# Kernel tuning notes

Measured on AMD Instinct MI355X. Metric: run time of the kernel, lower is better.

Reference implementation:

```python
import jax, jax.numpy as jnp
import numpy as np


def _coord1d(n):
    # make_coord: grid-center coordinates in (-1, 1)
    return -1.0 + 1.0 / n + (2.0 / n) * jnp.arange(n, dtype=jnp.float32)


def _conv1x1(x, w, b):
    # 1x1 conv == channel matmul. x: [B,C,H,W], w: [O,C], b: [O]
    return jnp.einsum('bchw,oc->bohw', x, w) + b[None, :, None, None]


def setup_inputs() -> dict:
    key = jax.random.key(0)
    ks = jax.random.split(key, 8)
    B, C, h, w = 2, 64, 96, 96
    d = 256
    Cin = (C + 2) * 4 + 2  # 266
    s = lambda k, shp, fan: (jax.random.normal(k, shp, jnp.float32) / np.sqrt(fan)).astype(jnp.float32)
    return {
        'feat': jax.random.normal(ks[0], (B, C, h, w), jnp.float32),
        'w00': s(ks[1], (d, Cin), Cin), 'b00': jnp.zeros((d,), jnp.float32),
        'w1': s(ks[2], (d, d), d), 'b1': jnp.zeros((d,), jnp.float32),
        'w2': s(ks[3], (3, d), d), 'b2': jnp.zeros((3,), jnp.float32),
        'ws1': s(ks[4], (C, C), C), 'bs1': jnp.zeros((C,), jnp.float32),
        'ws2': s(ks[5], (3, C), C), 'bs2': jnp.zeros((3,), jnp.float32),
        'target_h': 384, 'target_w': 384,
    }


def reference(feat, w00, b00, w1, b1, w2, b2, ws1, bs1, ws2, bs2, target_h, target_w):
    B, C, h, w = feat.shape
    H, W = int(target_h), int(target_w)
    # HR query coordinates, shared across batch. cy along height (dim0), cx along width (dim1)
    cy = jnp.broadcast_to(_coord1d(H)[:, None], (H, W))
    cx = jnp.broadcast_to(_coord1d(W)[None, :], (H, W))
    rx = 1.0 / h  # = 2/h/2, half-pixel radius along height
    ry = 1.0 / w
    eps_shift = 1e-6

    def nearest(c, n):
        # grid_sample nearest, align_corners=False: unnormalize then round (half-to-even, as nearbyint)
        u = ((c + 1.0) * n - 1.0) / 2.0
        return jnp.clip(jnp.round(u).astype(jnp.int32), 0, n - 1)

    rel_coords, feat_s, areas = [], [], []
    for vx in (-1.0, 1.0):
        for vy in (-1.0, 1.0):
            sy = jnp.clip(cy + vx * rx + eps_shift, -1.0 + 1e-6, 1.0 - 1e-6)
            sx = jnp.clip(cx + vy * ry + eps_shift, -1.0 + 1e-6, 1.0 - 1e-6)
            iy = nearest(sy, h)  # [H,W]
            ix = nearest(sx, w)
            feat_s.append(feat[:, :, iy, ix])  # [B,C,H,W] gather
            # nearest-sampled LR pixel-center coords (what grid_sample(pos_lr,...) returns)
            old_y = -1.0 + 1.0 / h + (2.0 / h) * iy.astype(jnp.float32)
            old_x = -1.0 + 1.0 / w + (2.0 / w) * ix.astype(jnp.float32)
            rel_y = (cy - old_y) * h
            rel_x = (cx - old_x) * w
            rel_coords.append(jnp.stack([rel_y, rel_x], 0))  # [2,H,W]
            areas.append(jnp.abs(rel_y * rel_x) + 1e-9)

    tot = areas[0] + areas[1] + areas[2] + areas[3]
    # LIIF area swap: 0<->3, 1<->2
    areas = [areas[3], areas[2], areas[1], areas[0]]
    feat_s = [f * (a / tot)[None, None] for f, a in zip(feat_s, areas)]

    scale_h, scale_w = H / h, W / w
    cell_h = (2.0 / H) * max(scale_h / 4.0, 1.0) * h
    cell_w = (2.0 / W) * max(scale_w / 4.0, 1.0) * w
    rel_cell = jnp.broadcast_to(
        jnp.array([cell_h, cell_w], jnp.float32)[None, :, None, None], (B, 2, H, W))
    rels = jnp.broadcast_to(jnp.concatenate(rel_coords, 0)[None], (B, 8, H, W))
    grid = jnp.concatenate([rels, *feat_s, rel_cell], axis=1)  # [B,266,H,W]

    x = _conv1x1(grid, w00, b00)
    ret = _conv1x1(jax.nn.gelu(_conv1x1(x, w1, b1), approximate=False), w2, b2)

    # shortcut branch: 1x1 MLP on LR feat, then bilinear border sample at coord
    sc = _conv1x1(jax.nn.relu(_conv1x1(feat, ws1, bs1)), ws2, bs2)  # [B,3,h,w]
    uy = ((cy + 1.0) * h - 1.0) / 2.0
    ux = ((cx + 1.0) * w - 1.0) / 2.0
    y0 = jnp.floor(uy)
    x0 = jnp.floor(ux)
    wy = uy - y0
    wx = ux - x0
    y0i = jnp.clip(y0.astype(jnp.int32), 0, h - 1)
    y1i = jnp.clip(y0.astype(jnp.int32) + 1, 0, h - 1)
    x0i = jnp.clip(x0.astype(jnp.int32), 0, w - 1)
    x1i = jnp.clip(x0.astype(jnp.int32) + 1, 0, w - 1)
    samp = (sc[:, :, y0i, x0i] * ((1 - wy) * (1 - wx))[None, None]
            + sc[:, :, y0i, x1i] * ((1 - wy) * wx)[None, None]
            + sc[:, :, y1i, x0i] * (wy * (1 - wx))[None, None]
            + sc[:, :, y1i, x1i] * (wy * wx)[None, None])
    return ret + samp
```

## Files before the change

kernel.cpp:

```cpp
#include <hip/hip_runtime.h>

typedef __bf16 bf16x8 __attribute__((ext_vector_type(8)));
typedef __bf16 bf16x4 __attribute__((ext_vector_type(4)));
typedef float f32x4 __attribute__((ext_vector_type(4)));

namespace {
constexpr int Bn = 2, Cn = 64, hn = 96, wn = 96, Hn = 384, Wn = 384;
constexpr int CIN = 266;
constexpr int TM = 64;
constexpr int SP = 296;
constexpr int L1_FRAGS = 9 * 16 * 64;
constexpr int L2_FRAGS = 8 * 16 * 64;
constexpr int L3_FRAGS = 8 * 64;
constexpr int N_FRAGS = L1_FRAGS + L2_FRAGS + L3_FRAGS;
constexpr int SC_OFF_BYTES = N_FRAGS * 16;
constexpr int B1EFF_OFF_BYTES = SC_OFF_BYTES + Bn * 3 * hn * wn * 4;
constexpr int FRAG_BLOCKS = N_FRAGS / 256;
constexpr int NPIX = Bn * hn * wn;
constexpr int SC_BLOCKS = NPIX / 256;
}

__global__ void prep_all(const float* __restrict__ w00, const float* __restrict__ w1,
                         const float* __restrict__ w2, const float* __restrict__ b00,
                         const float* __restrict__ b1,
                         const float* __restrict__ feat, const float* __restrict__ ws1,
                         const float* __restrict__ bs1, const float* __restrict__ ws2,
                         const float* __restrict__ bs2,
                         __bf16* __restrict__ wb, float* __restrict__ b1eff,
                         float* __restrict__ sc)
{
    const int bid = blockIdx.x;
    if (bid < FRAG_BLOCKS) {
        const int f = bid * 256 + threadIdx.x;
        bf16x8 v;
        if (f < L1_FRAGS) {
            const int k0 = f >> 10;
            const int mb = (f >> 6) & 15;
            const int l  = f & 63;
            const int m  = mb * 16 + (l & 15);
            const int kb = k0 * 32 + (l >> 4) * 8;
#pragma unroll
            for (int j = 0; j < 8; j++)
                v[j] = (kb + j < CIN) ? (__bf16)w00[m * CIN + kb + j] : (__bf16)0.f;
        } else if (f < L1_FRAGS + L2_FRAGS) {
            const int g = f - L1_FRAGS;
            const int k0 = g >> 10;
            const int mb = (g >> 6) & 15;
            const int l  = g & 63;
            const int m  = mb * 16 + (l & 15);
            const int kb = k0 * 32 + (l >> 4) * 8;
#pragma unroll
            for (int j = 0; j < 8; j++) v[j] = (__bf16)w1[m * 256 + kb + j];
        } else {
            const int g = f - (L1_FRAGS + L2_FRAGS);
            const int k0 = g >> 6;
            const int l  = g & 63;
            const int m  = l & 15;
            const int kb = k0 * 32 + (l >> 4) * 8;
#pragma unroll
            for (int j = 0; j < 8; j++)
                v[j] = (m < 3) ? (__bf16)w2[m * 256 + kb + j] : (__bf16)0.f;
        }
        *(bf16x8*)(wb + f * 8) = v;
        return;
    }
    if (bid == FRAG_BLOCKS) {
        __shared__ float cb[256];
        const int o = threadIdx.x;
        cb[o] = b00[o] + 0.5f * (w00[o * CIN + 264] + w00[o * CIN + 265]);
        __syncthreads();
        float v = b1[o];
#pragma unroll 4
        for (int k = 0; k < 256; k++) v = fmaf(w1[o * 256 + k], cb[k], v);
        b1eff[o] = v;
        return;
    }
    const int t = (bid - FRAG_BLOCKS - 1) * 256 + threadIdx.x;
    if (t >= NPIX) return;
    const int b = t / (hn * wn);
    const int yx = t % (hn * wn);
    const float* fp = feat + b * Cn * hn * wn + yx;
    float f[Cn];
#pragma unroll
    for (int c = 0; c < Cn; c++) f[c] = fp[c * hn * wn];
    float o0 = bs2[0], o1 = bs2[1], o2 = bs2[2];
#pragma unroll 1
    for (int co = 0; co < Cn; co += 4) {
        float v0 = bs1[co], v1 = bs1[co + 1], v2 = bs1[co + 2], v3 = bs1[co + 3];
        const float* wr = ws1 + co * Cn;
#pragma unroll
        for (int ci = 0; ci < Cn; ci++) {
            const float fv = f[ci];
            v0 = fmaf(wr[ci], fv, v0);
            v1 = fmaf(wr[Cn + ci], fv, v1);
            v2 = fmaf(wr[2 * Cn + ci], fv, v2);
            v3 = fmaf(wr[3 * Cn + ci], fv, v3);
        }
        v0 = fmaxf(v0, 0.f); v1 = fmaxf(v1, 0.f); v2 = fmaxf(v2, 0.f); v3 = fmaxf(v3, 0.f);
#pragma unroll
        for (int u = 0; u < 4; u++) {
            const float vv = (u == 0) ? v0 : (u == 1) ? v1 : (u == 2) ? v2 : v3;
            o0 = fmaf(ws2[co + u], vv, o0);
            o1 = fmaf(ws2[Cn + co + u], vv, o1);
            o2 = fmaf(ws2[2 * Cn + co + u], vv, o2);
        }
    }
    sc[(b * 3 + 0) * hn * wn + yx] = o0;
    sc[(b * 3 + 1) * hn * wn + yx] = o1;
    sc[(b * 3 + 2) * hn * wn + yx] = o2;
}

__device__ __forceinline__ float gelu_fast(float x) {
    const float d0 = -2.302118074f;
    const float d1 = -0.1029453754f;
    float t = x * x;
    float a = x * fmaf(t, d1, d0);
    float e = __builtin_amdgcn_exp2f(a);
    return x * __builtin_amdgcn_rcpf(1.f + e);
}

__device__ __forceinline__ bf16x4 pack4(f32x4 x) {
    bf16x4 v;
    v[0] = (__bf16)x[0]; v[1] = (__bf16)x[1]; v[2] = (__bf16)x[2]; v[3] = (__bf16)x[3];
    return v;
}


#define MF(A, B, C) __builtin_amdgcn_mfma_f32_16x16x32_bf16((A), (B), (C), 0, 0, 0)

#define GSTEP(k0, W0, W1) do {                                                  \
    const bf16x8 g0 = *(const bf16x8*)&Abuf[     lane16][(k0) * 32 + quad * 8]; \
    const bf16x8 g1 = *(const bf16x8*)&Abuf[16 + lane16][(k0) * 32 + quad * 8]; \
    const bf16x8 g2 = *(const bf16x8*)&Abuf[32 + lane16][(k0) * 32 + quad * 8]; \
    const bf16x8 g3 = *(const bf16x8*)&Abuf[48 + lane16][(k0) * 32 + quad * 8]; \
    a00 = MF(W0, g0, a00); a01 = MF(W1, g0, a01);                               \
    a10 = MF(W0, g1, a10); a11 = MF(W1, g1, a11);                               \
    a20 = MF(W0, g2, a20); a21 = MF(W1, g2, a21);                               \
    a30 = MF(W0, g3, a30); a31 = MF(W1, g3, a31);                               \
} while (0)

#define LDW(W0, W1, src, kk) do {                       \
    W0 = (src)[((kk) * 16 + mb0 + 0) * 64 + lane];      \
    W1 = (src)[((kk) * 16 + mb0 + 1) * 64 + lane];      \
} while (0)

__global__ __launch_bounds__(512, 4) void liif_main(
    const float* __restrict__ feat, const float* __restrict__ b1eff,
    const float* __restrict__ b2v, const __bf16* __restrict__ wb,
    const float* __restrict__ sc, float* __restrict__ out)
{
    __shared__ __align__(16) __bf16 Abuf[TM][SP];

    const int t = threadIdx.x;
    const int wv = t >> 6;
    const int lane = t & 63;
    const int lane16 = lane & 15;
    const int quad = lane >> 4;
    const int mb0 = wv * 2;

    constexpr int NWG = Bn * Hn * (Wn / TM);
    const int lt = (blockIdx.x & 7) * (NWG / 8) + (blockIdx.x >> 3);
    constexpr int TPR = Wn / TM;
    const int tx = lt % TPR;
    const int Y = (lt / TPR) % Hn;
    const int b = lt / (TPR * Hn);
    const int X0 = tx * TM;

    const float cy = -1.f + 1.f / Hn + (2.f / Hn) * (float)Y;

    const bf16x8* wf1 = (const bf16x8*)wb;
    const bf16x8* wf2 = wf1 + L1_FRAGS;
    const bf16x8* w2f = wf1 + (L1_FRAGS + L2_FRAGS);

    {
        const int p = lane;
        const int j = wv & 3;
        const int half = wv >> 2;
        const int X = X0 + p;
        const float cx = -1.f + 1.f / Wn + (2.f / Wn) * (float)X;
        float rely[4], relx[4], area[4];
        int iyv[4], ixv[4];
#pragma unroll
        for (int c = 0; c < 4; c++) {
            const float vx = (c & 2) ? 1.f : -1.f;
            const float vy = (c & 1) ? 1.f : -1.f;
            float sy = fminf(fmaxf(cy + vx * (1.f / hn) + 1e-6f, -1.f + 1e-6f), 1.f - 1e-6f);
            float sx = fminf(fmaxf(cx + vy * (1.f / wn) + 1e-6f, -1.f + 1e-6f), 1.f - 1e-6f);
            float uy = ((sy + 1.f) * hn - 1.f) * 0.5f;
            float ux = ((sx + 1.f) * wn - 1.f) * 0.5f;
            int iy = min(max((int)rintf(uy), 0), hn - 1);
            int ix = min(max((int)rintf(ux), 0), wn - 1);
            float oy = -1.f + 1.f / hn + (2.f / hn) * (float)iy;
            float ox = -1.f + 1.f / wn + (2.f / wn) * (float)ix;
            rely[c] = (cy - oy) * hn;
            relx[c] = (cx - ox) * wn;
            area[c] = fabsf(rely[c] * relx[c]) + 1e-9f;
            iyv[c] = iy; ixv[c] = ix;
        }
        const float tot = area[0] + area[1] + area[2] + area[3];
        const float wj = area[3 - j] / tot;

        if (wv == 0) {
            bf16x8 v;
#pragma unroll
            for (int c = 0; c < 4; c++) { v[2 * c] = (__bf16)rely[c]; v[2 * c + 1] = (__bf16)relx[c]; }
            *(bf16x8*)&Abuf[p][0] = v;
        }
        const float* fb = feat + ((b * Cn + half * 32) * hn + iyv[j]) * wn + ixv[j];
#pragma unroll
        for (int c8 = 0; c8 < 4; c8++) {
            bf16x8 v;
#pragma unroll
            for (int cc = 0; cc < 8; cc++)
                v[cc] = (__bf16)(fb[(c8 * 8 + cc) * (hn * wn)] * wj);
            *(bf16x8*)&Abuf[p][8 + 64 * j + half * 32 + c8 * 8] = v;
        }
        if (wv == 3) {
            bf16x8 z;
#pragma unroll
            for (int cc = 0; cc < 8; cc++) z[cc] = (__bf16)0.f;
            *(bf16x8*)&Abuf[p][264] = z;
            *(bf16x8*)&Abuf[p][272] = z;
            *(bf16x8*)&Abuf[p][280] = z;
        }
    }

    bf16x8 wE0, wE1, wO0, wO1;
    LDW(wE0, wE1, wf1, 0);
    LDW(wO0, wO1, wf1, 1);
    __syncthreads();

    const f32x4 zf = (f32x4){0.f, 0.f, 0.f, 0.f};
    f32x4 a00, a01, a10, a11, a20, a21, a30, a31;
    a00 = zf; a01 = zf; a10 = zf; a11 = zf; a20 = zf; a21 = zf; a30 = zf; a31 = zf;

    GSTEP(0, wE0, wE1); LDW(wE0, wE1, wf1, 2);
    GSTEP(1, wO0, wO1); LDW(wO0, wO1, wf1, 3);
    GSTEP(2, wE0, wE1); LDW(wE0, wE1, wf1, 4);
    GSTEP(3, wO0, wO1); LDW(wO0, wO1, wf1, 5);
    GSTEP(4, wE0, wE1); LDW(wE0, wE1, wf1, 6);
    GSTEP(5, wO0, wO1); LDW(wO0, wO1, wf1, 7);
    GSTEP(6, wE0, wE1); LDW(wE0, wE1, wf1, 8);
    GSTEP(7, wO0, wO1); LDW(wO0, wO1, wf2, 0);
    GSTEP(8, wE0, wE1); LDW(wE0, wE1, wf2, 1);

    __syncthreads();
    {
        const int ch0 = mb0 * 16 + quad * 4;
        *(bf16x4*)&Abuf[     lane16][ch0     ] = pack4(a00);
        *(bf16x4*)&Abuf[16 + lane16][ch0     ] = pack4(a10);
        *(bf16x4*)&Abuf[32 + lane16][ch0     ] = pack4(a20);
        *(bf16x4*)&Abuf[48 + lane16][ch0     ] = pack4(a30);
        *(bf16x4*)&Abuf[     lane16][ch0 + 16] = pack4(a01);
        *(bf16x4*)&Abuf[16 + lane16][ch0 + 16] = pack4(a11);
        *(bf16x4*)&Abuf[32 + lane16][ch0 + 16] = pack4(a21);
        *(bf16x4*)&Abuf[48 + lane16][ch0 + 16] = pack4(a31);
    }
    __syncthreads();

    a00 = zf; a01 = zf; a10 = zf; a11 = zf; a20 = zf; a21 = zf; a30 = zf; a31 = zf;

    GSTEP(0, wO0, wO1); LDW(wO0, wO1, wf2, 2);
    GSTEP(1, wE0, wE1); LDW(wE0, wE1, wf2, 3);
    GSTEP(2, wO0, wO1); LDW(wO0, wO1, wf2, 4);
    GSTEP(3, wE0, wE1); LDW(wE0, wE1, wf2, 5);
    GSTEP(4, wO0, wO1); LDW(wO0, wO1, wf2, 6);
    GSTEP(5, wE0, wE1); LDW(wE0, wE1, wf2, 7);
    GSTEP(6, wO0, wO1); wO0 = w2f[0 * 64 + lane];
    GSTEP(7, wE0, wE1); wE0 = w2f[1 * 64 + lane];

    __syncthreads();
    {
        const int ch0 = mb0 * 16 + quad * 4;
        const f32x4 bi0 = *(const f32x4*)&b1eff[ch0];
        const f32x4 bi1 = *(const f32x4*)&b1eff[ch0 + 16];
#define GEL4(x, bi) { bf16x4 v; v[0] = (__bf16)gelu_fast((x)[0] + (bi)[0]); \
        v[1] = (__bf16)gelu_fast((x)[1] + (bi)[1]); \
        v[2] = (__bf16)gelu_fast((x)[2] + (bi)[2]); \
        v[3] = (__bf16)gelu_fast((x)[3] + (bi)[3]); vv = v; }
        bf16x4 vv;
        GEL4(a00, bi0); *(bf16x4*)&Abuf[     lane16][ch0     ] = vv;
        GEL4(a10, bi0); *(bf16x4*)&Abuf[16 + lane16][ch0     ] = vv;
        GEL4(a20, bi0); *(bf16x4*)&Abuf[32 + lane16][ch0     ] = vv;
        GEL4(a30, bi0); *(bf16x4*)&Abuf[48 + lane16][ch0     ] = vv;
        GEL4(a01, bi1); *(bf16x4*)&Abuf[     lane16][ch0 + 16] = vv;
        GEL4(a11, bi1); *(bf16x4*)&Abuf[16 + lane16][ch0 + 16] = vv;
        GEL4(a21, bi1); *(bf16x4*)&Abuf[32 + lane16][ch0 + 16] = vv;
        GEL4(a31, bi1); *(bf16x4*)&Abuf[48 + lane16][ch0 + 16] = vv;
#undef GEL4
    }
    __syncthreads();

    if (wv < 4) {
        f32x4 acc3 = zf;
#define YF(k0) (*(const bf16x8*)&Abuf[wv * 16 + lane16][(k0) * 32 + quad * 8])
        acc3 = MF(wO0, YF(0), acc3); wO0 = w2f[2 * 64 + lane];
        acc3 = MF(wE0, YF(1), acc3); wE0 = w2f[3 * 64 + lane];
        acc3 = MF(wO0, YF(2), acc3); wO0 = w2f[4 * 64 + lane];
        acc3 = MF(wE0, YF(3), acc3); wE0 = w2f[5 * 64 + lane];
        acc3 = MF(wO0, YF(4), acc3); wO0 = w2f[6 * 64 + lane];
        acc3 = MF(wE0, YF(5), acc3); wE0 = w2f[7 * 64 + lane];
        acc3 = MF(wO0, YF(6), acc3);
        acc3 = MF(wE0, YF(7), acc3);
#undef YF

        if (quad == 0) {
            const int pix = wv * 16 + lane16;
            const int X = X0 + pix;
            const float uy = ((cy + 1.f) * hn - 1.f) * 0.5f;
            const float fy = floorf(uy);
            const float wy = uy - fy;
            const int y0i = min(max((int)fy, 0), hn - 1);
            const int y1i = min(max((int)fy + 1, 0), hn - 1);
            const float cx = -1.f + 1.f / Wn + (2.f / Wn) * (float)X;
            const float ux = ((cx + 1.f) * wn - 1.f) * 0.5f;
            const float fx = floorf(ux);
            const float wx = ux - fx;
            const int x0i = min(max((int)fx, 0), wn - 1);
            const int x1i = min(max((int)fx + 1, 0), wn - 1);
            const float w00b = (1.f - wy) * (1.f - wx), w01b = (1.f - wy) * wx;
            const float w10b = wy * (1.f - wx), w11b = wy * wx;
#pragma unroll
            for (int r = 0; r < 3; r++) {
                const float* scb = sc + (b * 3 + r) * (hn * wn);
                const float samp = scb[y0i * wn + x0i] * w00b + scb[y0i * wn + x1i] * w01b
                                 + scb[y1i * wn + x0i] * w10b + scb[y1i * wn + x1i] * w11b;
                out[((b * 3 + r) * Hn + Y) * Wn + X] = acc3[r] + b2v[r] + samp;
            }
        }
    }
}

extern "C" void kernel_launch(void* const* d_in, const int* in_sizes, int n_in,
                              void* d_out, int out_size, void* d_ws, size_t ws_size,
                              hipStream_t stream)
{
    const float* feat = (const float*)d_in[0];
    const float* w00  = (const float*)d_in[1];
    const float* b00  = (const float*)d_in[2];
    const float* w1   = (const float*)d_in[3];
    const float* b1   = (const float*)d_in[4];
    const float* w2   = (const float*)d_in[5];
    const float* b2   = (const float*)d_in[6];
    const float* ws1  = (const float*)d_in[7];
    const float* bs1  = (const float*)d_in[8];
    const float* ws2  = (const float*)d_in[9];
    const float* bs2  = (const float*)d_in[10];
    float* out = (float*)d_out;

    __bf16* wb    = (__bf16*)d_ws;
    float* scbuf  = (float*)((char*)d_ws + SC_OFF_BYTES);
    float* b1eff  = (float*)((char*)d_ws + B1EFF_OFF_BYTES);

    prep_all<<<FRAG_BLOCKS + 1 + SC_BLOCKS, 256, 0, stream>>>(
        w00, w1, w2, b00, b1, feat, ws1, bs1, ws2, bs2, wb, b1eff, scbuf);
    liif_main<<<Bn * Hn * (Wn / TM), 512, 0, stream>>>(feat, b1eff, b2, wb, scbuf, out);
}
```

Before: 209.6 us.

## Switch MLP GEMMs to 32x32x16 MFMA with 4 waves and XOR-swizzled LDS

Replaces the 16x16x32 bf16 MFMA tiling with 32x32x16 MFMA tiles and repacks the weight fragments to match. The workgroup shrinks from 8 waves to 4, so each wave covers 64 output channels over the 64-pixel tile. The LDS activation buffer gets an XOR swizzle keyed on row to reduce bank conflicts, and the first weight fragments are loaded before the gather phase. The larger MFMA shape is meant to raise math throughput per instruction and cut LDS reads per FLOP. In exchange each thread holds more accumulator registers, occupancy changes, and each wave does twice the gather work.

Result: no change. 208.6 us (-0.5%).

```diff
diff --git a/kernel.cpp b/kernel.cpp
--- a/kernel.cpp
+++ b/kernel.cpp
@@ -3,14 +3,15 @@
 typedef __bf16 bf16x8 __attribute__((ext_vector_type(8)));
 typedef __bf16 bf16x4 __attribute__((ext_vector_type(4)));
 typedef float f32x4 __attribute__((ext_vector_type(4)));
+typedef float f32x16 __attribute__((ext_vector_type(16)));
 
 namespace {
 constexpr int Bn = 2, Cn = 64, hn = 96, wn = 96, Hn = 384, Wn = 384;
 constexpr int CIN = 266;
 constexpr int TM = 64;
 constexpr int SP = 296;
-constexpr int L1_FRAGS = 9 * 16 * 64;
-constexpr int L2_FRAGS = 8 * 16 * 64;
+constexpr int L1_FRAGS = 18 * 8 * 64;
+constexpr int L2_FRAGS = 16 * 8 * 64;
 constexpr int L3_FRAGS = 8 * 64;
 constexpr int N_FRAGS = L1_FRAGS + L2_FRAGS + L3_FRAGS;
 constexpr int SC_OFF_BYTES = N_FRAGS * 16;
@@ -34,21 +35,21 @@
         const int f = bid * 256 + threadIdx.x;
         bf16x8 v;
         if (f < L1_FRAGS) {
-            const int k0 = f >> 10;
-            const int mb = (f >> 6) & 15;
+            const int k0 = f >> 9;
+            const int ob = (f >> 6) & 7;
             const int l  = f & 63;
-            const int m  = mb * 16 + (l & 15);
-            const int kb = k0 * 32 + (l >> 4) * 8;
+            const int m  = ob * 32 + (l & 31);
+            const int kb = k0 * 16 + (l >> 5) * 8;
 #pragma unroll
             for (int j = 0; j < 8; j++)
                 v[j] = (kb + j < CIN) ? (__bf16)w00[m * CIN + kb + j] : (__bf16)0.f;
         } else if (f < L1_FRAGS + L2_FRAGS) {
             const int g = f - L1_FRAGS;
-            const int k0 = g >> 10;
-            const int mb = (g >> 6) & 15;
+            const int k0 = g >> 9;
+            const int ob = (g >> 6) & 7;
             const int l  = g & 63;
-            const int m  = mb * 16 + (l & 15);
-            const int kb = k0 * 32 + (l >> 4) * 8;
+            const int m  = ob * 32 + (l & 31);
+            const int kb = k0 * 16 + (l >> 5) * 8;
 #pragma unroll
             for (int j = 0; j < 8; j++) v[j] = (__bf16)w1[m * 256 + kb + j];
         } else {
@@ -119,32 +120,46 @@
     return x * __builtin_amdgcn_rcpf(1.f + e);
 }
 
-__device__ __forceinline__ bf16x4 pack4(f32x4 x) {
-    bf16x4 v;
-    v[0] = (__bf16)x[0]; v[1] = (__bf16)x[1]; v[2] = (__bf16)x[2]; v[3] = (__bf16)x[3];
+__device__ __forceinline__ bf16x4 pk4(float a, float b, float c, float d) {
+    bf16x4 v; v[0] = (__bf16)a; v[1] = (__bf16)b; v[2] = (__bf16)c; v[3] = (__bf16)d;
     return v;
 }
 
 
-#define MF(A, B, C) __builtin_amdgcn_mfma_f32_16x16x32_bf16((A), (B), (C), 0, 0, 0)
-
-#define GSTEP(k0, W0, W1) do {                                                  \
-    const bf16x8 g0 = *(const bf16x8*)&Abuf[     lane16][(k0) * 32 + quad * 8]; \
-    const bf16x8 g1 = *(const bf16x8*)&Abuf[16 + lane16][(k0) * 32 + quad * 8]; \
-    const bf16x8 g2 = *(const bf16x8*)&Abuf[32 + lane16][(k0) * 32 + quad * 8]; \
-    const bf16x8 g3 = *(const bf16x8*)&Abuf[48 + lane16][(k0) * 32 + quad * 8]; \
-    a00 = MF(W0, g0, a00); a01 = MF(W1, g0, a01);                               \
-    a10 = MF(W0, g1, a10); a11 = MF(W1, g1, a11);                               \
-    a20 = MF(W0, g2, a20); a21 = MF(W1, g2, a21);                               \
-    a30 = MF(W0, g3, a30); a31 = MF(W1, g3, a31);                               \
+#define MF32(A, B, C) __builtin_amdgcn_mfma_f32_32x32x16_bf16((A), (B), (C), 0, 0, 0)
+#define MF16(A, B, C) __builtin_amdgcn_mfma_f32_16x16x32_bf16((A), (B), (C), 0, 0, 0)
+
+#define GS(k0, W0, W1) do {                                                     \
+    const int pc = (((2 * (k0) + hi) ^ skey) * 8);                              \
+    const bf16x8 g0 = *(const bf16x8*)&Abuf[     lane31][pc];                   \
+    const bf16x8 g1 = *(const bf16x8*)&Abuf[32 + lane31][pc];                   \
+    c00 = MF32(W0, g0, c00); c01 = MF32(W1, g0, c01);                           \
+    c10 = MF32(W0, g1, c10); c11 = MF32(W1, g1, c11);                           \
 } while (0)
 
-#define LDW(W0, W1, src, kk) do {                       \
-    W0 = (src)[((kk) * 16 + mb0 + 0) * 64 + lane];      \
-    W1 = (src)[((kk) * 16 + mb0 + 1) * 64 + lane];      \
+#define LW(W0, W1, src, kk) do {                        \
+    W0 = (src)[((kk) * 8 + ob0 + 0) * 64 + lane];       \
+    W1 = (src)[((kk) * 8 + ob0 + 1) * 64 + lane];       \
 } while (0)
 
-__global__ __launch_bounds__(512, 4) void liif_main(
+#define EP1(ACC, OB, ROW) do {                                                          \
+    *(bf16x4*)&Abuf[ROW][(((OB) * 4 + 0) ^ skey) * 8 + hi * 4] = pk4((ACC)[0], (ACC)[1], (ACC)[2], (ACC)[3]);     \
+    *(bf16x4*)&Abuf[ROW][(((OB) * 4 + 1) ^ skey) * 8 + hi * 4] = pk4((ACC)[4], (ACC)[5], (ACC)[6], (ACC)[7]);     \
+    *(bf16x4*)&Abuf[ROW][(((OB) * 4 + 2) ^ skey) * 8 + hi * 4] = pk4((ACC)[8], (ACC)[9], (ACC)[10], (ACC)[11]);   \
+    *(bf16x4*)&Abuf[ROW][(((OB) * 4 + 3) ^ skey) * 8 + hi * 4] = pk4((ACC)[12], (ACC)[13], (ACC)[14], (ACC)[15]); \
+} while (0)
+
+#define EP2G(A0, A1, OB, G) do {                                                        \
+    const f32x4 bi = *(const f32x4*)&b1eff[(OB) * 32 + 8 * (G) + hi * 4];               \
+    *(bf16x4*)&Abuf[     lane31][(((OB) * 4 + (G)) ^ skey) * 8 + hi * 4] =              \
+        pk4(gelu_fast((A0)[4*(G)+0] + bi[0]), gelu_fast((A0)[4*(G)+1] + bi[1]),         \
+            gelu_fast((A0)[4*(G)+2] + bi[2]), gelu_fast((A0)[4*(G)+3] + bi[3]));        \
+    *(bf16x4*)&Abuf[32 + lane31][(((OB) * 4 + (G)) ^ skey) * 8 + hi * 4] =              \
+        pk4(gelu_fast((A1)[4*(G)+0] + bi[0]), gelu_fast((A1)[4*(G)+1] + bi[1]),         \
+            gelu_fast((A1)[4*(G)+2] + bi[2]), gelu_fast((A1)[4*(G)+3] + bi[3]));        \
+} while (0)
+
+__global__ __launch_bounds__(256, 3) void liif_main(
     const float* __restrict__ feat, const float* __restrict__ b1eff,
     const float* __restrict__ b2v, const __bf16* __restrict__ wb,
     const float* __restrict__ sc, float* __restrict__ out)
@@ -154,9 +169,12 @@
     const int t = threadIdx.x;
     const int wv = t >> 6;
     const int lane = t & 63;
+    const int lane31 = lane & 31;
+    const int hi = lane >> 5;
+    const int skey = (lane31 >> 3) & 3;
     const int lane16 = lane & 15;
     const int quad = lane >> 4;
-    const int mb0 = wv * 2;
+    const int ob0 = wv * 2;
 
     constexpr int NWG = Bn * Hn * (Wn / TM);
     const int lt = (blockIdx.x & 7) * (NWG / 8) + (blockIdx.x >> 3);
@@ -172,10 +190,16 @@
     const bf16x8* wf2 = wf1 + L1_FRAGS;
     const bf16x8* w2f = wf1 + (L1_FRAGS + L2_FRAGS);
 
+    bf16x8 wP00, wP01, wP10, wP11, wP20, wP21, wP30, wP31;
+    LW(wP00, wP01, wf1, 0);
+    LW(wP10, wP11, wf1, 1);
+    LW(wP20, wP21, wf1, 2);
+    LW(wP30, wP31, wf1, 3);
+
     {
         const int p = lane;
-        const int j = wv & 3;
-        const int half = wv >> 2;
+        const int j = wv;
+        const int pkey = (p >> 3) & 3;
         const int X = X0 + p;
         const float cx = -1.f + 1.f / Wn + (2.f / Wn) * (float)X;
         float rely[4], relx[4], area[4];
@@ -200,133 +224,130 @@
         const float tot = area[0] + area[1] + area[2] + area[3];
         const float wj = area[3 - j] / tot;
 
-        if (wv == 0) {
+        if (j == 0) {
             bf16x8 v;
 #pragma unroll
             for (int c = 0; c < 4; c++) { v[2 * c] = (__bf16)rely[c]; v[2 * c + 1] = (__bf16)relx[c]; }
-            *(bf16x8*)&Abuf[p][0] = v;
-        }
-        const float* fb = feat + ((b * Cn + half * 32) * hn + iyv[j]) * wn + ixv[j];
-#pragma unroll
-        for (int c8 = 0; c8 < 4; c8++) {
+            *(bf16x8*)&Abuf[p][(0 ^ pkey) * 8] = v;
+        }
+        const float* fb = feat + ((b * Cn) * hn + iyv[j]) * wn + ixv[j];
+#pragma unroll
+        for (int c8 = 0; c8 < 8; c8++) {
             bf16x8 v;
 #pragma unroll
             for (int cc = 0; cc < 8; cc++)
                 v[cc] = (__bf16)(fb[(c8 * 8 + cc) * (hn * wn)] * wj);
-            *(bf16x8*)&Abuf[p][8 + 64 * j + half * 32 + c8 * 8] = v;
-        }
-        if (wv == 3) {
+            *(bf16x8*)&Abuf[p][((1 + 8 * j + c8) ^ pkey) * 8] = v;
+        }
+        if (j == 3) {
             bf16x8 z;
 #pragma unroll
             for (int cc = 0; cc < 8; cc++) z[cc] = (__bf16)0.f;
-            *(bf16x8*)&Abuf[p][264] = z;
-            *(bf16x8*)&Abuf[p][272] = z;
-            *(bf16x8*)&Abuf[p][280] = z;
-        }
-    }
-
-    bf16x8 wE0, wE1, wO0, wO1;
-    LDW(wE0, wE1, wf1, 0);
-    LDW(wO0, wO1, wf1, 1);
-    __syncthreads();
-
-    const f32x4 zf = (f32x4){0.f, 0.f, 0.f, 0.f};
-    f32x4 a00, a01, a10, a11, a20, a21, a30, a31;
-    a00 = zf; a01 = zf; a10 = zf; a11 = zf; a20 = zf; a21 = zf; a30 = zf; a31 = zf;
-
-    GSTEP(0, wE0, wE1); LDW(wE0, wE1, wf1, 2);
-    GSTEP(1, wO0, wO1); LDW(wO0, wO1, wf1, 3);
-    GSTEP(2, wE0, wE1); LDW(wE0, wE1, wf1, 4);
-    GSTEP(3, wO0, wO1); LDW(wO0, wO1, wf1, 5);
-    GSTEP(4, wE0, wE1); LDW(wE0, wE1, wf1, 6);
-    GSTEP(5, wO0, wO1); LDW(wO0, wO1, wf1, 7);
-    GSTEP(6, wE0, wE1); LDW(wE0, wE1, wf1, 8);
-    GSTEP(7, wO0, wO1); LDW(wO0, wO1, wf2, 0);
-    GSTEP(8, wE0, wE1); LDW(wE0, wE1, wf2, 1);
-
-    __syncthreads();
+            *(bf16x8*)&Abuf[p][(33 ^ pkey) * 8] = z;
+            *(bf16x8*)&Abuf[p][(34 ^ pkey) * 8] = z;
+            *(bf16x8*)&Abuf[p][(35 ^ pkey) * 8] = z;
+        }
+    }
+    __syncthreads();
+
+    const f32x16 zf16 = (f32x16)(0.f);
+    f32x16 c00, c01, c10, c11;
+    c00 = zf16; c01 = zf16; c10 = zf16; c11 = zf16;
+
+    GS(0,  wP00, wP01); LW(wP00, wP01, wf1, 4);
+    GS(1,  wP10, wP11); LW(wP10, wP11, wf1, 5);
+    GS(2,  wP20, wP21); LW(wP20, wP21, wf1, 6);
+    GS(3,  wP30, wP31); LW(wP30, wP31, wf1, 7);
+    GS(4,  wP00, wP01); LW(wP00, wP01, wf1, 8);
+    GS(5,  wP10, wP11); LW(wP10, wP11, wf1, 9);
+    GS(6,  wP20, wP21); LW(wP20, wP21, wf1, 10);
+    GS(7,  wP30, wP31); LW(wP30, wP31, wf1, 11);
+    GS(8,  wP00, wP01); LW(wP00, wP01, wf1, 12);
+    GS(9,  wP10, wP11); LW(wP10, wP11, wf1, 13);
+    GS(10, wP20, wP21); LW(wP20, wP21, wf1, 14);
+    GS(11, wP30, wP31); LW(wP30, wP31, wf1, 15);
+    GS(12, wP00, wP01); LW(wP00, wP01, wf1, 16);
+    GS(13, wP10, wP11); LW(wP10, wP11, wf1, 17);
+    GS(14, wP20, wP21); LW(wP20, wP21, wf2, 0);
+    GS(15, wP30, wP31); LW(wP30, wP31, wf2, 1);
+    GS(16, wP00, wP01); LW(wP00, wP01, wf2, 2);
+    GS(17, wP10, wP11); LW(wP10, wP11, wf2, 3);
+
+    __syncthreads();
+    EP1(c00, ob0,     lane31);
+    EP1(c01, ob0 + 1, lane31);
+    EP1(c10, ob0,     32 + lane31);
+    EP1(c11, ob0 + 1, 32 + lane31);
+    __syncthreads();
+
+    c00 = zf16; c01 = zf16; c10 = zf16; c11 = zf16;
+
+    GS(0,  wP20, wP21); LW(wP20, wP21, wf2, 4);
+    GS(1,  wP30, wP31); LW(wP30, wP31, wf2, 5);
+    GS(2,  wP00, wP01); LW(wP00, wP01, wf2, 6);
+    GS(3,  wP10, wP11); LW(wP10, wP11, wf2, 7);
+    GS(4,  wP20, wP21); LW(wP20, wP21, wf2, 8);
+    GS(5,  wP30, wP31); LW(wP30, wP31, wf2, 9);
+    GS(6,  wP00, wP01); LW(wP00, wP01, wf2, 10);
+    GS(7,  wP10, wP11); LW(wP10, wP11, wf2, 11);
+    GS(8,  wP20, wP21); LW(wP20, wP21, wf2, 12);
+    GS(9,  wP30, wP31); LW(wP30, wP31, wf2, 13);
+    GS(10, wP00, wP01); LW(wP00, wP01, wf2, 14);
+    GS(11, wP10, wP11); LW(wP10, wP11, wf2, 15);
+    GS(12, wP20, wP21); wP20 = w2f[0 * 64 + lane];
+    GS(13, wP30, wP31); wP30 = w2f[1 * 64 + lane];
+    GS(14, wP00, wP01); wP00 = w2f[2 * 64 + lane];
+    GS(15, wP10, wP11); wP10 = w2f[3 * 64 + lane];
+
+    __syncthreads();
+    EP2G(c00, c10, ob0,     0);
+    EP2G(c00, c10, ob0,     1);
+    EP2G(c00, c10, ob0,     2);
+    EP2G(c00, c10, ob0,     3);
+    EP2G(c01, c11, ob0 + 1, 0);
+    EP2G(c01, c11, ob0 + 1, 1);
+    EP2G(c01, c11, ob0 + 1, 2);
+    EP2G(c01, c11, ob0 + 1, 3);
+    __syncthreads();
+
+    f32x4 acc3 = (f32x4){0.f, 0.f, 0.f, 0.f};
     {
-        const int ch0 = mb0 * 16 + quad * 4;
-        *(bf16x4*)&Abuf[     lane16][ch0     ] = pack4(a00);
-        *(bf16x4*)&Abuf[16 + lane16][ch0     ] = pack4(a10);
-        *(bf16x4*)&Abuf[32 + lane16][ch0     ] = pack4(a20);
-        *(bf16x4*)&Abuf[48 + lane16][ch0     ] = pack4(a30);
-        *(bf16x4*)&Abuf[     lane16][ch0 + 16] = pack4(a01);
-        *(bf16x4*)&Abuf[16 + lane16][ch0 + 16] = pack4(a11);
-        *(bf16x4*)&Abuf[32 + lane16][ch0 + 16] = pack4(a21);
-        *(bf16x4*)&Abuf[48 + lane16][ch0 + 16] = pack4(a31);
-    }
-    __syncthreads();
-
-    a00 = zf; a01 = zf; a10 = zf; a11 = zf; a20 = zf; a21 = zf; a30 = zf; a31 = zf;
-
-    GSTEP(0, wO0, wO1); LDW(wO0, wO1, wf2, 2);
-    GSTEP(1, wE0, wE1); LDW(wE0, wE1, wf2, 3);
-    GSTEP(2, wO0, wO1); LDW(wO0, wO1, wf2, 4);
-    GSTEP(3, wE0, wE1); LDW(wE0, wE1, wf2, 5);
-    GSTEP(4, wO0, wO1); LDW(wO0, wO1, wf2, 6);
-    GSTEP(5, wE0, wE1); LDW(wE0, wE1, wf2, 7);
-    GSTEP(6, wO0, wO1); wO0 = w2f[0 * 64 + lane];
-    GSTEP(7, wE0, wE1); wE0 = w2f[1 * 64 + lane];
-
-    __syncthreads();
-    {
-        const int ch0 = mb0 * 16 + quad * 4;
-        const f32x4 bi0 = *(const f32x4*)&b1eff[ch0];
-        const f32x4 bi1 = *(const f32x4*)&b1eff[ch0 + 16];
-#define GEL4(x, bi) { bf16x4 v; v[0] = (__bf16)gelu_fast((x)[0] + (bi)[0]); \
-        v[1] = (__bf16)gelu_fast((x)[1] + (bi)[1]); \
-        v[2] = (__bf16)gelu_fast((x)[2] + (bi)[2]); \
-        v[3] = (__bf16)gelu_fast((x)[3] + (bi)[3]); vv = v; }
-        bf16x4 vv;
-        GEL4(a00, bi0); *(bf16x4*)&Abuf[     lane16][ch0     ] = vv;
-        GEL4(a10, bi0); *(bf16x4*)&Abuf[16 + lane16][ch0     ] = vv;
-        GEL4(a20, bi0); *(bf16x4*)&Abuf[32 + lane16][ch0     ] = vv;
-        GEL4(a30, bi0); *(bf16x4*)&Abuf[48 + lane16][ch0     ] = vv;
-        GEL4(a01, bi1); *(bf16x4*)&Abuf[     lane16][ch0 + 16] = vv;
-        GEL4(a11, bi1); *(bf16x4*)&Abuf[16 + lane16][ch0 + 16] = vv;
-        GEL4(a21, bi1); *(bf16x4*)&Abuf[32 + lane16][ch0 + 16] = vv;
-        GEL4(a31, bi1); *(bf16x4*)&Abuf[48 + lane16][ch0 + 16] = vv;
-#undef GEL4
-    }
-    __syncthreads();
-
-    if (wv < 4) {
-        f32x4 acc3 = zf;
-#define YF(k0) (*(const bf16x8*)&Abuf[wv * 16 + lane16][(k0) * 32 + quad * 8])
-        acc3 = MF(wO0, YF(0), acc3); wO0 = w2f[2 * 64 + lane];
-        acc3 = MF(wE0, YF(1), acc3); wE0 = w2f[3 * 64 + lane];
-        acc3 = MF(wO0, YF(2), acc3); wO0 = w2f[4 * 64 + lane];
-        acc3 = MF(wE0, YF(3), acc3); wE0 = w2f[5 * 64 + lane];
-        acc3 = MF(wO0, YF(4), acc3); wO0 = w2f[6 * 64 + lane];
-        acc3 = MF(wE0, YF(5), acc3); wE0 = w2f[7 * 64 + lane];
-        acc3 = MF(wO0, YF(6), acc3);
-        acc3 = MF(wE0, YF(7), acc3);
+        const int row3 = wv * 16 + lane16;
+        const int key3 = (row3 >> 3) & 3;
+#define YF(k0) (*(const bf16x8*)&Abuf[row3][(((k0) * 4 + quad) ^ key3) * 8])
+        acc3 = MF16(wP20, YF(0), acc3); wP20 = w2f[4 * 64 + lane];
+        acc3 = MF16(wP30, YF(1), acc3); wP30 = w2f[5 * 64 + lane];
+        acc3 = MF16(wP00, YF(2), acc3); wP00 = w2f[6 * 64 + lane];
+        acc3 = MF16(wP10, YF(3), acc3); wP10 = w2f[7 * 64 + lane];
+        acc3 = MF16(wP20, YF(4), acc3);
+        acc3 = MF16(wP30, YF(5), acc3);
+        acc3 = MF16(wP00, YF(6), acc3);
+        acc3 = MF16(wP10, YF(7), acc3);
 #undef YF
-
-        if (quad == 0) {
-            const int pix = wv * 16 + lane16;
-            const int X = X0 + pix;
-            const float uy = ((cy + 1.f) * hn - 1.f) * 0.5f;
-            const float fy = floorf(uy);
-            const float wy = uy - fy;
-            const int y0i = min(max((int)fy, 0), hn - 1);
-            const int y1i = min(max((int)fy + 1, 0), hn - 1);
-            const float cx = -1.f + 1.f / Wn + (2.f / Wn) * (float)X;
-            const float ux = ((cx + 1.f) * wn - 1.f) * 0.5f;
-            const float fx = floorf(ux);
-            const float wx = ux - fx;
-            const int x0i = min(max((int)fx, 0), wn - 1);
-            const int x1i = min(max((int)fx + 1, 0), wn - 1);
-            const float w00b = (1.f - wy) * (1.f - wx), w01b = (1.f - wy) * wx;
-            const float w10b = wy * (1.f - wx), w11b = wy * wx;
-#pragma unroll
-            for (int r = 0; r < 3; r++) {
-                const float* scb = sc + (b * 3 + r) * (hn * wn);
-                const float samp = scb[y0i * wn + x0i] * w00b + scb[y0i * wn + x1i] * w01b
-                                 + scb[y1i * wn + x0i] * w10b + scb[y1i * wn + x1i] * w11b;
-                out[((b * 3 + r) * Hn + Y) * Wn + X] = acc3[r] + b2v[r] + samp;
-            }
+    }
+
+    if (quad == 0) {
+        const int pix = wv * 16 + lane16;
+        const int X = X0 + pix;
+        const float uy = ((cy + 1.f) * hn - 1.f) * 0.5f;
+        const float fy = floorf(uy);
+        const float wy = uy - fy;
+        const int y0i = min(max((int)fy, 0), hn - 1);
+        const int y1i = min(max((int)fy + 1, 0), hn - 1);
+        const float cx = -1.f + 1.f / Wn + (2.f / Wn) * (float)X;
+        const float ux = ((cx + 1.f) * wn - 1.f) * 0.5f;
+        const float fx = floorf(ux);
+        const float wx = ux - fx;
+        const int x0i = min(max((int)fx, 0), wn - 1);
+        const int x1i = min(max((int)fx + 1, 0), wn - 1);
+        const float w00b = (1.f - wy) * (1.f - wx), w01b = (1.f - wy) * wx;
+        const float w10b = wy * (1.f - wx), w11b = wy * wx;
+#pragma unroll
+        for (int r = 0; r < 3; r++) {
+            const float* scb = sc + (b * 3 + r) * (hn * wn);
+            const float samp = scb[y0i * wn + x0i] * w00b + scb[y0i * wn + x1i] * w01b
+                             + scb[y1i * wn + x0i] * w10b + scb[y1i * wn + x1i] * w11b;
+            out[((b * 3 + r) * Hn + Y) * Wn + X] = acc3[r] + b2v[r] + samp;
         }
     }
 }
@@ -354,5 +375,5 @@
 
     prep_all<<<FRAG_BLOCKS + 1 + SC_BLOCKS, 256, 0, stream>>>(
         w00, w1, w2, b00, b1, feat, ws1, bs1, ws2, bs2, wb, b1eff, scbuf);
-    liif_main<<<Bn * Hn * (Wn / TM), 512, 0, stream>>>(feat, b1eff, b2, wb, scbuf, out);
-}
+    liif_main<<<Bn * Hn * (Wn / TM), 256, 0, stream>>>(feat, b1eff, b2, wb, scbuf, out);
+}
```
